# Performance work log

Measured on AMD Instinct MI355X. Metric: run time of the kernel, lower is better.

The kernel has to match this reference:

```python
import jax, jax.numpy as jnp
import numpy as np

H = 768
NH = 12
DH = H // NH  # 64


def setup_inputs() -> dict:
    key = jax.random.key(0)
    ks = jax.random.split(key, 20)
    s = 1.0 / np.sqrt(H)
    def lin(k, din, dout):
        kw, kb = jax.random.split(k)
        W = jax.random.uniform(kw, (din, dout), jnp.float32, -s, s)
        b = jax.random.uniform(kb, (dout,), jnp.float32, -s, s)
        return W, b
    Wq, bq = lin(ks[0], H, H)
    Wk, bk = lin(ks[1], H, H)
    Wv, bv = lin(ks[2], H, H)
    Wt, bt = lin(ks[3], H, H)
    Wi, bi = lin(ks[4], H, H)
    W1, b1 = lin(ks[5], H, H)
    W2, b2 = lin(ks[6], H, 1)
    text = jax.random.normal(ks[7], (8, 64, H), jnp.float32)
    image = jax.random.normal(ks[8], (8, 197, H), jnp.float32)
    return dict(text=text, image=image, Wq=Wq, bq=bq, Wk=Wk, bk=bk, Wv=Wv, bv=bv,
                Wt=Wt, bt=bt, Wi=Wi, bi=bi, W1=W1, b1=b1, W2=W2, b2=b2)


def reference(text, image, Wq, bq, Wk, bk, Wv, bv, Wt, bt, Wi, bi, W1, b1, W2, b2):
    bsz, t_len, _ = text.shape
    i_len = image.shape[1]
    # relevance gate MLP on broadcast product
    text_emb = text @ Wt + bt          # [b, t, H]
    image_emb = image @ Wi + bi        # [b, i, H]
    rel = text_emb[:, :, None, :] * image_emb[:, None, :, :]  # [b, t, i, H]
    rel = jax.nn.relu(rel @ W1 + b1)
    gate = jax.nn.sigmoid(rel @ W2 + b2)  # [b, t, i, 1]
    gate = gate.reshape(bsz, 1, t_len, i_len)
    # cross-attention
    def heads(x, L):
        return x.reshape(bsz, L, NH, DH).transpose(0, 2, 1, 3)  # [b, h, L, dh]
    q = heads(text @ Wq + bq, t_len)
    k = heads(image @ Wk + bk, i_len)
    v = heads(image @ Wv + bv, i_len)
    scores = jnp.einsum('bhtd,bhid->bhti', q, k) / np.sqrt(DH)
    probs = jax.nn.softmax(scores, axis=-1) * gate   # [b, h, t, i]
    ctx = jnp.einsum('bhti,bhid->bhtd', probs, v)    # [b, h, t, dh]
    return ctx.transpose(0, 2, 1, 3).reshape(bsz, t_len, H)
```

## Files before the change

### kernel.cpp

```cpp
#include <hip/hip_runtime.h>
#include <stdint.h>

#define HD 768
#define NHEADS 12
#define DHEAD 64
#define BATCH 8
#define TLEN 64
#define ILEN 197
#define NPAIRS 100864
#define MTILES 394

typedef __attribute__((ext_vector_type(8))) short short8;
typedef __attribute__((ext_vector_type(4))) float f32x4;

__device__ __forceinline__ short f2bf(float x) {
    union { float f; uint32_t u; } v; v.f = x;
    uint32_t r = v.u + 0x7FFFu + ((v.u >> 16) & 1u);
    return (short)(r >> 16);
}
__device__ __forceinline__ float bf2f(short s) {
    union { uint32_t u; float f; } v; v.u = ((uint32_t)(unsigned short)s) << 16;
    return v.f;
}
__device__ __forceinline__ void gll16(const void* g, void* l) {
    __builtin_amdgcn_global_load_lds(
        (const __attribute__((address_space(1))) unsigned int*)g,
        (__attribute__((address_space(3))) unsigned int*)l, 16, 0, 0);
}

__global__ __launch_bounds__(256) void prep_weights(
    const float* __restrict__ Wq, const float* __restrict__ Wk,
    const float* __restrict__ Wv, const float* __restrict__ Wt,
    const float* __restrict__ Wi, const float* __restrict__ W1,
    short* __restrict__ W5s, short* __restrict__ W1Bs)
{
    __shared__ float tile[64][65];
    int bx = blockIdx.x;
    int tid = threadIdx.x;
    if (bx >= 720) {
        int idx = bx - 720;
        int pn = idx / 12, kt = idx - pn * 12;
        int c = tid;
        int j = pn * 256 + c;
        char* dst = (char*)W1Bs + (size_t)idx * 32768 + c * 128;
        int swz = (c & 7) << 4;
#pragma unroll
        for (int kg = 0; kg < 8; ++kg) {
            short8 o;
#pragma unroll
            for (int e = 0; e < 8; ++e)
                o[e] = f2bf(W1[(size_t)(kt * 64 + kg * 8 + e) * HD + j]);
            *(short8*)(dst + ((kg * 16) ^ swz)) = o;
        }
        return;
    }
    int seg = bx / 144, ti = bx - seg * 144;
    const float* src = (seg == 0) ? Wt : (seg == 1) ? Wq : (seg == 2) ? Wi
                     : (seg == 3) ? Wk : Wv;
    int kt = ti / 12, ntile = ti - kt * 12;
#pragma unroll
    for (int pass = 0; pass < 16; ++pass) {
        int idx = pass * 256 + tid;
        int kk = idx >> 6, nn = idx & 63;
        tile[kk][nn] = src[(size_t)(kt * 64 + kk) * HD + ntile * 64 + nn];
    }
    __syncthreads();
    size_t base = ((size_t)(seg * 12 + ntile) * 12 + kt) * 8192;
#pragma unroll
    for (int pass = 0; pass < 16; ++pass) {
        int idx = pass * 256 + tid;
        int col = idx >> 6, kloc = idx & 63;
        float x = tile[kloc][col];
        short h = f2bf(x);
        short lw = f2bf(x - bf2f(h));
        int sidx = (col * 64 + kloc) ^ ((col & 7) << 3);
        W5s[base + sidx] = h;
        W5s[base + 4096 + sidx] = lw;
    }
}

__global__ __launch_bounds__(256, 1) void proj_kernel(
    const float* __restrict__ X, int M,
    const short* __restrict__ W5s, int segbase,
    const float* __restrict__ bias0, const float* __restrict__ bias1,
    const float* __restrict__ bias2,
    float* __restrict__ out0, float* __restrict__ out1, float* __restrict__ out2)
{
    __shared__ __align__(16) short Bs[2][8192];
    int tid = threadIdx.x;
    int l = tid & 63, w = tid >> 6;
    int lo = l & 15, grp = l >> 4;
    int y = blockIdx.y;
    int segl = y / 12, ntile = y - segl * 12;
    int seg = segbase + segl;
    const char* wsrc = (const char*)W5s + (size_t)((seg * 12 + ntile) * 12) * 16384;
    {
        const char* s = wsrc + w * 4096 + l * 16;
        char* d = (char*)&Bs[0][0] + w * 4096;
        gll16(s, d); gll16(s + 1024, d + 1024);
        gll16(s + 2048, d + 2048); gll16(s + 3072, d + 3072);
    }
    int arow = blockIdx.x * 64 + w * 16 + lo;
    bool aok = arow < M;
    const float* xrow = X + (size_t)(aok ? arow : 0) * HD;
    short8 ah[24], al[24];
#pragma unroll
    for (int kc = 0; kc < 24; ++kc) {
        int kb = kc * 32 + grp * 8;
        float4 xa = {0.f, 0.f, 0.f, 0.f}, xb = {0.f, 0.f, 0.f, 0.f};
        if (aok) { xa = *(const float4*)(xrow + kb); xb = *(const float4*)(xrow + kb + 4); }
        float xs[8] = {xa.x, xa.y, xa.z, xa.w, xb.x, xb.y, xb.z, xb.w};
#pragma unroll
        for (int e = 0; e < 8; ++e) {
            short hh = f2bf(xs[e]);
            ah[kc][e] = hh;
            al[kc][e] = f2bf(xs[e] - bf2f(hh));
        }
    }
    __syncthreads();

    f32x4 acc[4];
    f32x4 z4 = {0.f, 0.f, 0.f, 0.f};
#pragma unroll
    for (int js = 0; js < 4; ++js) acc[js] = z4;

#pragma unroll
    for (int kk = 0; kk < 12; ++kk) {
        const short* buf = &Bs[kk & 1][0];
        if (kk < 11) {
            const char* s = wsrc + (size_t)(kk + 1) * 16384 + w * 4096 + l * 16;
            char* d = (char*)&Bs[(kk + 1) & 1][0] + w * 4096;
            gll16(s, d); gll16(s + 1024, d + 1024);
            gll16(s + 2048, d + 2048); gll16(s + 3072, d + 3072);
            asm volatile("s_waitcnt vmcnt(4)" ::: "memory");
        } else {
            asm volatile("s_waitcnt vmcnt(0)" ::: "memory");
        }
        __builtin_amdgcn_s_barrier();
        asm volatile("" ::: "memory");
#pragma unroll
        for (int js = 0; js < 4; ++js) {
            int col = js * 16 + lo;
            int base = col * 64;
            int sw = (col & 7) << 3;
#pragma unroll
            for (int kcl = 0; kcl < 2; ++kcl) {
                int idx = (base + kcl * 32 + grp * 8) ^ sw;
                short8 bh = *(const short8*)&buf[idx];
                short8 bl = *(const short8*)&buf[4096 + idx];
                int kc = kk * 2 + kcl;
                acc[js] = __builtin_amdgcn_mfma_f32_16x16x32_bf16(ah[kc], bh, acc[js], 0, 0, 0);
                acc[js] = __builtin_amdgcn_mfma_f32_16x16x32_bf16(ah[kc], bl, acc[js], 0, 0, 0);
                acc[js] = __builtin_amdgcn_mfma_f32_16x16x32_bf16(al[kc], bh, acc[js], 0, 0, 0);
            }
        }
        asm volatile("s_waitcnt lgkmcnt(0)" ::: "memory");
        __builtin_amdgcn_s_barrier();
        asm volatile("" ::: "memory");
    }
    const float* bp = (segl == 0) ? bias0 : (segl == 1) ? bias1 : bias2;
    float* op = (segl == 0) ? out0 : (segl == 1) ? out1 : out2;
#pragma unroll
    for (int js = 0; js < 4; ++js) {
        int cc = ntile * 64 + js * 16 + lo;
        float bvv = bp[cc];
#pragma unroll
        for (int r = 0; r < 4; ++r) {
            int orow = blockIdx.x * 64 + w * 16 + grp * 4 + r;
            if (orow < M) op[(size_t)orow * HD + cc] = acc[js][r] + bvv;
        }
    }
}

__global__ __launch_bounds__(256) void build_a(
    const float* __restrict__ te, const float* __restrict__ ie,
    short* __restrict__ As, int mstart)
{
    int bx = blockIdx.x;
    int m_l = bx / 12, kt = bx - m_l * 12;
    int tid = threadIdx.x;
    int p = (mstart + m_l) * 256 + tid;
    int b = p / 12608; int rr = p - b * 12608;
    int t = rr / 197;  int i = rr - t * 197;
    const float* tp = te + (size_t)(b * 64 + t) * HD + kt * 64;
    const float* ip = ie + (size_t)(b * 197 + i) * HD + kt * 64;
    char* dst = (char*)As + ((size_t)(m_l * 12 + kt) * 32768) + tid * 128;
    int swz = (tid & 7) << 4;
#pragma unroll
    for (int kg = 0; kg < 8; ++kg) {
        float4 xa = *(const float4*)(ip + kg * 8);
        float4 xb = *(const float4*)(ip + kg * 8 + 4);
        float4 ta = *(const float4*)(tp + kg * 8);
        float4 tb = *(const float4*)(tp + kg * 8 + 4);
        short8 o;
        o[0] = f2bf(xa.x * ta.x); o[1] = f2bf(xa.y * ta.y);
        o[2] = f2bf(xa.z * ta.z); o[3] = f2bf(xa.w * ta.w);
        o[4] = f2bf(xb.x * tb.x); o[5] = f2bf(xb.y * tb.y);
        o[6] = f2bf(xb.z * tb.z); o[7] = f2bf(xb.w * tb.w);
        *(short8*)(dst + ((kg * 16) ^ swz)) = o;
    }
}

__global__ __launch_bounds__(512, 2) void gate_gemm(
    const short* __restrict__ As, const short* __restrict__ W1Bs,
    const float* __restrict__ b1, const float* __restrict__ W2,
    float* __restrict__ plg, int mstart)
{
    __shared__ __align__(16) char lds[131072];
    int tid = threadIdx.x;
    int lane = tid & 63, wid = tid >> 6;
    int lo = lane & 15, grp = lane >> 4;
    int wr = wid >> 2, wc = wid & 2 ? (wid & 3) : (wid & 3);
    wc = wid & 3;
    int bx0 = blockIdx.x;
    int nwg = gridDim.x;
    int qq = nwg >> 3, rr8 = nwg & 7;
    int xcd = bx0 & 7;
    int logical = (xcd < rr8 ? xcd * (qq + 1) : rr8 * (qq + 1) + (xcd - rr8) * qq)
                + (bx0 >> 3);
    int m_l = logical / 3, pn = logical - m_l * 3;

    const char* Ag = (const char*)As + (size_t)m_l * 12 * 32768;
    const char* Bg = (const char*)W1Bs + (size_t)pn * 12 * 32768;

    {
        gll16(Ag + tid * 16,          lds + tid * 16);
        gll16(Ag + 8192 + tid * 16,   lds + 8192 + tid * 16);
        gll16(Ag + 16384 + tid * 16,  lds + 16384 + tid * 16);
        gll16(Ag + 24576 + tid * 16,  lds + 24576 + tid * 16);
        gll16(Bg + tid * 16,          lds + 65536 + tid * 16);
        gll16(Bg + 8192 + tid * 16,   lds + 65536 + 8192 + tid * 16);
        gll16(Bg + 16384 + tid * 16,  lds + 65536 + 16384 + tid * 16);
        gll16(Bg + 24576 + tid * 16,  lds + 65536 + 24576 + tid * 16);
    }

    f32x4 acc[8][4];
    f32x4 z4 = {0.f, 0.f, 0.f, 0.f};
#pragma unroll
    for (int rt = 0; rt < 8; ++rt)
#pragma unroll
        for (int ct = 0; ct < 4; ++ct) acc[rt][ct] = z4;
    int swz = (lo & 7) << 4;

    for (int kt = 0; kt < 12; ++kt) {
        int par = kt & 1, npar = par ^ 1;
        int aoff = par * 32768;
        int boff = 65536 + par * 32768;
        bool more = kt < 11;

        asm volatile("s_waitcnt vmcnt(0)" ::: "memory");
        __builtin_amdgcn_s_barrier();
        asm volatile("" ::: "memory");

        if (more) {
            const char* Aun = Ag + (size_t)(kt + 1) * 32768;
            const char* Bun = Bg + (size_t)(kt + 1) * 32768;
            int dA = npar * 32768, dB = 65536 + npar * 32768;
            gll16(Aun + tid * 16,          lds + dA + tid * 16);
            gll16(Aun + 8192 + tid * 16,   lds + dA + 8192 + tid * 16);
            gll16(Aun + 16384 + tid * 16,  lds + dA + 16384 + tid * 16);
            gll16(Aun + 24576 + tid * 16,  lds + dA + 24576 + tid * 16);
            gll16(Bun + tid * 16,          lds + dB + tid * 16);
            gll16(Bun + 8192 + tid * 16,   lds + dB + 8192 + tid * 16);
            gll16(Bun + 16384 + tid * 16,  lds + dB + 16384 + tid * 16);
            gll16(Bun + 24576 + tid * 16,  lds + dB + 24576 + tid * 16);
        }

        short8 bfr[4][2];
#pragma unroll
        for (int ct = 0; ct < 4; ++ct) {
            int c = wc * 64 + ct * 16 + lo;
#pragma unroll
            for (int ks = 0; ks < 2; ++ks)
                bfr[ct][ks] = *(const short8*)(lds + boff + c * 128 + ((ks * 64 + grp * 16) ^ swz));
        }
#pragma unroll
        for (int q = 0; q < 4; ++q) {
            short8 af[2][2];
#pragma unroll
            for (int i2 = 0; i2 < 2; ++i2) {
                int r = wr * 128 + (2 * q + i2) * 16 + lo;
#pragma unroll
                for (int ks = 0; ks < 2; ++ks)
                    af[i2][ks] = *(const short8*)(lds + aoff + r * 128 + ((ks * 64 + grp * 16) ^ swz));
            }
            __builtin_amdgcn_s_setprio(1);
#pragma unroll
            for (int i2 = 0; i2 < 2; ++i2)
#pragma unroll
                for (int ct = 0; ct < 4; ++ct)
#pragma unroll
                    for (int ks = 0; ks < 2; ++ks)
                        acc[2 * q + i2][ct] = __builtin_amdgcn_mfma_f32_16x16x32_bf16(
                            af[i2][ks], bfr[ct][ks], acc[2 * q + i2][ct], 0, 0, 0);
            __builtin_amdgcn_s_setprio(0);
        }
    }

    float b1v[4], w2v[4];
#pragma unroll
    for (int ct = 0; ct < 4; ++ct) {
        int j = pn * 256 + wc * 64 + ct * 16 + lo;
        b1v[ct] = b1[j]; w2v[ct] = W2[j];
    }
    float pl[8][4];
#pragma unroll
    for (int rt = 0; rt < 8; ++rt)
#pragma unroll
        for (int r = 0; r < 4; ++r) {
            float s = 0.f;
#pragma unroll
            for (int ct = 0; ct < 4; ++ct)
                s += fmaxf(acc[rt][ct][r] + b1v[ct], 0.f) * w2v[ct];
            pl[rt][r] = s;
        }
#pragma unroll
    for (int msk = 1; msk <= 8; msk <<= 1)
#pragma unroll
        for (int rt = 0; rt < 8; ++rt)
#pragma unroll
            for (int r = 0; r < 4; ++r)
                pl[rt][r] += __shfl_xor(pl[rt][r], msk);

    __syncthreads();
    float* red = (float*)lds;
    if (lo == 0) {
#pragma unroll
        for (int rt = 0; rt < 8; ++rt)
#pragma unroll
            for (int r = 0; r < 4; ++r)
                red[wid * 128 + rt * 16 + grp * 4 + r] = pl[rt][r];
    }
    __syncthreads();
    if (tid < 256) {
        int wr_ = tid >> 7, rl = tid & 127;
        float s = red[(wr_ * 4 + 0) * 128 + rl] + red[(wr_ * 4 + 1) * 128 + rl]
                + red[(wr_ * 4 + 2) * 128 + rl] + red[(wr_ * 4 + 3) * 128 + rl];
        plg[(size_t)pn * NPAIRS + (size_t)(mstart + m_l) * 256 + tid] = s;
    }
}

__global__ __launch_bounds__(256) void gate_fin(
    const float* __restrict__ plg, const float* __restrict__ b2,
    float* __restrict__ gateb)
{
    int idx = blockIdx.x * 256 + threadIdx.x;
    if (idx < NPAIRS) {
        float s = plg[idx] + plg[NPAIRS + idx] + plg[2 * NPAIRS + idx] + b2[0];
        gateb[idx] = 1.f / (1.f + __expf(-s));
    }
}

__global__ __launch_bounds__(256) void attn_kernel(
    const float* __restrict__ q, const float* __restrict__ k,
    const float* __restrict__ v, const float* __restrict__ gate,
    float* __restrict__ out)
{
    __shared__ float k_s[ILEN * 65];
    __shared__ float p_s[4][200];
    int bx = blockIdx.x;
    int tq = bx & 3;
    int h = (bx >> 2) % NHEADS;
    int b = bx / (4 * NHEADS);
    int tid = threadIdx.x;
    for (int idx = tid; idx < ILEN * DHEAD; idx += 256) {
        int i = idx >> 6, d = idx & 63;
        k_s[i * 65 + d] = k[(size_t)(b * ILEN + i) * HD + h * DHEAD + d];
    }
    __syncthreads();

    int l = tid & 63, w = tid >> 6;
    for (int tt = 0; tt < 4; ++tt) {
        int t = tq * 16 + w * 4 + tt;
        float qv = q[(size_t)(b * 64 + t) * HD + h * DHEAD + l];
        float s0 = 0.f, s1 = 0.f, s2 = 0.f, s3 = 0.f;
        int i0 = l, i1 = 64 + l, i2 = 128 + l;
        int i3c = (192 + l < ILEN) ? 192 + l : 0;
        for (int d = 0; d < 64; ++d) {
            float qd = __shfl(qv, d);
            s0 += qd * k_s[i0 * 65 + d];
            s1 += qd * k_s[i1 * 65 + d];
            s2 += qd * k_s[i2 * 65 + d];
            s3 += qd * k_s[i3c * 65 + d];
        }
        float sc[4] = {s0, s1, s2, s3};
        float m = -3.0e38f;
#pragma unroll
        for (int rep = 0; rep < 4; ++rep) {
            int i = rep * 64 + l;
            sc[rep] = (i < ILEN) ? sc[rep] * 0.125f : -3.0e38f;
            m = fmaxf(m, sc[rep]);
        }
        for (int mask = 32; mask >= 1; mask >>= 1) m = fmaxf(m, __shfl_xor(m, mask));
        float sum = 0.f;
#pragma unroll
        for (int rep = 0; rep < 4; ++rep) {
            float e = __expf(sc[rep] - m);
            sc[rep] = e;
            sum += e;
        }
        for (int mask = 32; mask >= 1; mask >>= 1) sum += __shfl_xor(sum, mask);
        float inv = 1.f / sum;
        const float* grow = gate + (size_t)(b * 64 + t) * ILEN;
#pragma unroll
        for (int rep = 0; rep < 4; ++rep) {
            int i = rep * 64 + l;
            if (i < 200) p_s[w][i] = (i < ILEN) ? sc[rep] * inv * grow[i] : 0.f;
        }
        float ctx = 0.f;
        const float* vbase = v + (size_t)(b * ILEN) * HD + h * DHEAD + l;
        for (int c = 0; c < 49; ++c) {
            float4 p4 = *(const float4*)&p_s[w][c * 4];
            ctx += p4.x * vbase[(size_t)(c * 4 + 0) * HD];
            ctx += p4.y * vbase[(size_t)(c * 4 + 1) * HD];
            ctx += p4.z * vbase[(size_t)(c * 4 + 2) * HD];
            ctx += p4.w * vbase[(size_t)(c * 4 + 3) * HD];
        }
        {
            float4 p4 = *(const float4*)&p_s[w][196];
            ctx += p4.x * vbase[(size_t)196 * HD];
        }
        out[(size_t)(b * 64 + t) * HD + h * DHEAD + l] = ctx;
    }
}

extern "C" void kernel_launch(void* const* d_in, const int* in_sizes, int n_in,
                              void* d_out, int out_size, void* d_ws, size_t ws_size,
                              hipStream_t stream)
{
    const float* text  = (const float*)d_in[0];
    const float* image = (const float*)d_in[1];
    const float* Wq = (const float*)d_in[2];
    const float* bq = (const float*)d_in[3];
    const float* Wk = (const float*)d_in[4];
    const float* bk = (const float*)d_in[5];
    const float* Wv = (const float*)d_in[6];
    const float* bv = (const float*)d_in[7];
    const float* Wt = (const float*)d_in[8];
    const float* bt = (const float*)d_in[9];
    const float* Wi = (const float*)d_in[10];
    const float* bi = (const float*)d_in[11];
    const float* W1 = (const float*)d_in[12];
    const float* b1 = (const float*)d_in[13];
    const float* W2 = (const float*)d_in[14];
    const float* b2 = (const float*)d_in[15];
    float* out = (float*)d_out;

    char* ws = (char*)d_ws;
    size_t off = 0;
    auto carve = [&](size_t bytes) -> void* {
        void* p = (void*)(ws + off);
        off += (bytes + 255) & ~(size_t)255;
        return p;
    };
    short* W5s  = (short*)carve((size_t)5 * 144 * 8192 * 2);
    short* W1Bs = (short*)carve((size_t)36 * 32768);
    float* te    = (float*)carve((size_t)512 * 768 * 4);
    float* qb    = (float*)carve((size_t)512 * 768 * 4);
    float* ieb   = (float*)carve((size_t)1576 * 768 * 4);
    float* kb    = (float*)carve((size_t)1576 * 768 * 4);
    float* vb    = (float*)carve((size_t)1576 * 768 * 4);
    float* gateb = (float*)carve((size_t)NPAIRS * 4);
    float* plg   = (float*)carve((size_t)3 * NPAIRS * 4);

    size_t per_m = (size_t)12 * 32768;
    size_t avail = (ws_size > off) ? (ws_size - off) : 0;
    int stripe = (int)(avail / per_m);
    if (stripe > MTILES) stripe = MTILES;
    if (stripe < 1) stripe = 1;
    short* As = (short*)(ws + off);
    int nst = (MTILES + stripe - 1) / stripe;

    hipLaunchKernelGGL(prep_weights, dim3(756), dim3(256), 0, stream,
                       Wq, Wk, Wv, Wt, Wi, W1, W5s, W1Bs);
    hipLaunchKernelGGL(proj_kernel, dim3(8, 24), dim3(256), 0, stream,
                       text, 512, W5s, 0, bt, bq, (const float*)nullptr,
                       te, qb, (float*)nullptr);
    hipLaunchKernelGGL(proj_kernel, dim3(25, 36), dim3(256), 0, stream,
                       image, 1576, W5s, 2, bi, bk, bv,
                       ieb, kb, vb);
    for (int s = 0; s < nst; ++s) {
        int m0 = s * stripe;
        int mc = (MTILES - m0 < stripe) ? (MTILES - m0) : stripe;
        hipLaunchKernelGGL(build_a, dim3(mc * 12), dim3(256), 0, stream,
                           te, ieb, As, m0);
        hipLaunchKernelGGL(gate_gemm, dim3(mc * 3), dim3(512), 0, stream,
                           As, W1Bs, b1, W2, plg, m0);
    }
    hipLaunchKernelGGL(gate_fin, dim3((NPAIRS + 255) / 256), dim3(256), 0, stream,
                       plg, b2, gateb);
    hipLaunchKernelGGL(attn_kernel, dim3(BATCH * NHEADS * 4), dim3(256), 0, stream,
                       qb, kb, vb, gateb, out);
}
```

Before: 389.1 us.

## Split gate GEMM K-tiles to 32 and use four-stage LDS prefetch pipeline

The gate GEMM's K tile goes from 64 to 32. The packed A and W1 buffers are re-laid out into 16 KB chunks with a matching 4-way swizzle, and the main loop uses a 4-slot ring buffer with three tiles in flight. Partial vmcnt waits replace the full drain, so global-to-LDS loads overlap with MFMA work instead of blocking each iteration. The trade-off is twice as many barriers, each covering half the MFMA work, plus changed layouts in prep_weights and build_a.

```diff
diff --git a/kernel.cpp b/kernel.cpp
--- a/kernel.cpp
+++ b/kernel.cpp
@@ -39,17 +39,17 @@
     int tid = threadIdx.x;
     if (bx >= 720) {
         int idx = bx - 720;
-        int pn = idx / 12, kt = idx - pn * 12;
+        int pn = idx / 24, kt = idx - pn * 24;
         int c = tid;
         int j = pn * 256 + c;
-        char* dst = (char*)W1Bs + (size_t)idx * 32768 + c * 128;
-        int swz = (c & 7) << 4;
-#pragma unroll
-        for (int kg = 0; kg < 8; ++kg) {
+        char* dst = (char*)W1Bs + (size_t)idx * 16384 + c * 64;
+        int swz = (c & 3) << 4;
+#pragma unroll
+        for (int kg = 0; kg < 4; ++kg) {
             short8 o;
 #pragma unroll
             for (int e = 0; e < 8; ++e)
-                o[e] = f2bf(W1[(size_t)(kt * 64 + kg * 8 + e) * HD + j]);
+                o[e] = f2bf(W1[(size_t)(kt * 32 + kg * 8 + e) * HD + j]);
             *(short8*)(dst + ((kg * 16) ^ swz)) = o;
         }
         return;
@@ -184,20 +184,24 @@
     int t = rr / 197;  int i = rr - t * 197;
     const float* tp = te + (size_t)(b * 64 + t) * HD + kt * 64;
     const float* ip = ie + (size_t)(b * 197 + i) * HD + kt * 64;
-    char* dst = (char*)As + ((size_t)(m_l * 12 + kt) * 32768) + tid * 128;
-    int swz = (tid & 7) << 4;
-#pragma unroll
-    for (int kg = 0; kg < 8; ++kg) {
-        float4 xa = *(const float4*)(ip + kg * 8);
-        float4 xb = *(const float4*)(ip + kg * 8 + 4);
-        float4 ta = *(const float4*)(tp + kg * 8);
-        float4 tb = *(const float4*)(tp + kg * 8 + 4);
-        short8 o;
-        o[0] = f2bf(xa.x * ta.x); o[1] = f2bf(xa.y * ta.y);
-        o[2] = f2bf(xa.z * ta.z); o[3] = f2bf(xa.w * ta.w);
-        o[4] = f2bf(xb.x * tb.x); o[5] = f2bf(xb.y * tb.y);
-        o[6] = f2bf(xb.z * tb.z); o[7] = f2bf(xb.w * tb.w);
-        *(short8*)(dst + ((kg * 16) ^ swz)) = o;
+    int swz = (tid & 3) << 4;
+#pragma unroll
+    for (int h = 0; h < 2; ++h) {
+        char* dst = (char*)As + ((size_t)(m_l * 24 + kt * 2 + h) * 16384) + tid * 64;
+#pragma unroll
+        for (int kg = 0; kg < 4; ++kg) {
+            int kb = h * 32 + kg * 8;
+            float4 xa = *(const float4*)(ip + kb);
+            float4 xb = *(const float4*)(ip + kb + 4);
+            float4 ta = *(const float4*)(tp + kb);
+            float4 tb = *(const float4*)(tp + kb + 4);
+            short8 o;
+            o[0] = f2bf(xa.x * ta.x); o[1] = f2bf(xa.y * ta.y);
+            o[2] = f2bf(xa.z * ta.z); o[3] = f2bf(xa.w * ta.w);
+            o[4] = f2bf(xb.x * tb.x); o[5] = f2bf(xb.y * tb.y);
+            o[6] = f2bf(xb.z * tb.z); o[7] = f2bf(xb.w * tb.w);
+            *(short8*)(dst + ((kg * 16) ^ swz)) = o;
+        }
     }
 }
 
@@ -210,8 +214,7 @@
     int tid = threadIdx.x;
     int lane = tid & 63, wid = tid >> 6;
     int lo = lane & 15, grp = lane >> 4;
-    int wr = wid >> 2, wc = wid & 2 ? (wid & 3) : (wid & 3);
-    wc = wid & 3;
+    int wr = wid >> 2, wc = wid & 3;
     int bx0 = blockIdx.x;
     int nwg = gridDim.x;
     int qq = nwg >> 3, rr8 = nwg & 7;
@@ -220,19 +223,19 @@
                 + (bx0 >> 3);
     int m_l = logical / 3, pn = logical - m_l * 3;
 
-    const char* Ag = (const char*)As + (size_t)m_l * 12 * 32768;
-    const char* Bg = (const char*)W1Bs + (size_t)pn * 12 * 32768;
-
-    {
-        gll16(Ag + tid * 16,          lds + tid * 16);
-        gll16(Ag + 8192 + tid * 16,   lds + 8192 + tid * 16);
-        gll16(Ag + 16384 + tid * 16,  lds + 16384 + tid * 16);
-        gll16(Ag + 24576 + tid * 16,  lds + 24576 + tid * 16);
-        gll16(Bg + tid * 16,          lds + 65536 + tid * 16);
-        gll16(Bg + 8192 + tid * 16,   lds + 65536 + 8192 + tid * 16);
-        gll16(Bg + 16384 + tid * 16,  lds + 65536 + 16384 + tid * 16);
-        gll16(Bg + 24576 + tid * 16,  lds + 65536 + 24576 + tid * 16);
-    }
+    const char* Ag = (const char*)As + (size_t)m_l * 24 * 16384;
+    const char* Bg = (const char*)W1Bs + (size_t)pn * 24 * 16384;
+
+    auto stage = [&](int tt) {
+        int s = (tt & 3) * 16384;
+        const char* sa = Ag + (size_t)tt * 16384 + tid * 16;
+        const char* sb = Bg + (size_t)tt * 16384 + tid * 16;
+        gll16(sa,        lds + s + tid * 16);
+        gll16(sa + 8192, lds + s + 8192 + tid * 16);
+        gll16(sb,        lds + 65536 + s + tid * 16);
+        gll16(sb + 8192, lds + 65536 + s + 8192 + tid * 16);
+    };
+    stage(0); stage(1); stage(2);
 
     f32x4 acc[8][4];
     f32x4 z4 = {0.f, 0.f, 0.f, 0.f};
@@ -240,59 +243,39 @@
     for (int rt = 0; rt < 8; ++rt)
 #pragma unroll
         for (int ct = 0; ct < 4; ++ct) acc[rt][ct] = z4;
-    int swz = (lo & 7) << 4;
-
-    for (int kt = 0; kt < 12; ++kt) {
-        int par = kt & 1, npar = par ^ 1;
-        int aoff = par * 32768;
-        int boff = 65536 + par * 32768;
-        bool more = kt < 11;
-
-        asm volatile("s_waitcnt vmcnt(0)" ::: "memory");
+    int swz = (lo & 3) << 4;
+
+    for (int k = 0; k < 24; ++k) {
+        if (k <= 21)      asm volatile("s_waitcnt vmcnt(8)" ::: "memory");
+        else if (k == 22) asm volatile("s_waitcnt vmcnt(4)" ::: "memory");
+        else              asm volatile("s_waitcnt vmcnt(0)" ::: "memory");
         __builtin_amdgcn_s_barrier();
         asm volatile("" ::: "memory");
-
-        if (more) {
-            const char* Aun = Ag + (size_t)(kt + 1) * 32768;
-            const char* Bun = Bg + (size_t)(kt + 1) * 32768;
-            int dA = npar * 32768, dB = 65536 + npar * 32768;
-            gll16(Aun + tid * 16,          lds + dA + tid * 16);
-            gll16(Aun + 8192 + tid * 16,   lds + dA + 8192 + tid * 16);
-            gll16(Aun + 16384 + tid * 16,  lds + dA + 16384 + tid * 16);
-            gll16(Aun + 24576 + tid * 16,  lds + dA + 24576 + tid * 16);
-            gll16(Bun + tid * 16,          lds + dB + tid * 16);
-            gll16(Bun + 8192 + tid * 16,   lds + dB + 8192 + tid * 16);
-            gll16(Bun + 16384 + tid * 16,  lds + dB + 16384 + tid * 16);
-            gll16(Bun + 24576 + tid * 16,  lds + dB + 24576 + tid * 16);
-        }
-
-        short8 bfr[4][2];
+        if (k + 3 < 24) stage(k + 3);
+
+        int sA = (k & 3) * 16384;
+        int sB = 65536 + (k & 3) * 16384;
+        short8 bfr[4];
 #pragma unroll
         for (int ct = 0; ct < 4; ++ct) {
             int c = wc * 64 + ct * 16 + lo;
-#pragma unroll
-            for (int ks = 0; ks < 2; ++ks)
-                bfr[ct][ks] = *(const short8*)(lds + boff + c * 128 + ((ks * 64 + grp * 16) ^ swz));
+            bfr[ct] = *(const short8*)(lds + sB + c * 64 + ((grp * 16) ^ swz));
         }
 #pragma unroll
         for (int q = 0; q < 4; ++q) {
-            short8 af[2][2];
+            short8 af[2];
 #pragma unroll
             for (int i2 = 0; i2 < 2; ++i2) {
                 int r = wr * 128 + (2 * q + i2) * 16 + lo;
-#pragma unroll
-                for (int ks = 0; ks < 2; ++ks)
-                    af[i2][ks] = *(const short8*)(lds + aoff + r * 128 + ((ks * 64 + grp * 16) ^ swz));
+                af[i2] = *(const short8*)(lds + sA + r * 64 + ((grp * 16) ^ swz));
             }
             __builtin_amdgcn_s_setprio(1);
 #pragma unroll
             for (int i2 = 0; i2 < 2; ++i2)
 #pragma unroll
                 for (int ct = 0; ct < 4; ++ct)
-#pragma unroll
-                    for (int ks = 0; ks < 2; ++ks)
-                        acc[2 * q + i2][ct] = __builtin_amdgcn_mfma_f32_16x16x32_bf16(
-                            af[i2][ks], bfr[ct][ks], acc[2 * q + i2][ct], 0, 0, 0);
+                    acc[2 * q + i2][ct] = __builtin_amdgcn_mfma_f32_16x16x32_bf16(
+                        af[i2], bfr[ct], acc[2 * q + i2][ct], 0, 0, 0);
             __builtin_amdgcn_s_setprio(0);
         }
     }
@@ -454,7 +437,7 @@
         return p;
     };
     short* W5s  = (short*)carve((size_t)5 * 144 * 8192 * 2);
-    short* W1Bs = (short*)carve((size_t)36 * 32768);
+    short* W1Bs = (short*)carve((size_t)72 * 16384);
     float* te    = (float*)carve((size_t)512 * 768 * 4);
     float* qb    = (float*)carve((size_t)512 * 768 * 4);
     float* ieb   = (float*)carve((size_t)1576 * 768 * 4);
@@ -463,7 +446,7 @@
     float* gateb = (float*)carve((size_t)NPAIRS * 4);
     float* plg   = (float*)carve((size_t)3 * NPAIRS * 4);
 
-    size_t per_m = (size_t)12 * 32768;
+    size_t per_m = (size_t)24 * 16384;
     size_t avail = (ws_size > off) ? (ws_size - off) : 0;
     int stripe = (int)(avail / per_m);
     if (stripe > MTILES) stripe = MTILES;
@@ -471,7 +454,7 @@
     short* As = (short*)(ws + off);
     int nst = (MTILES + stripe - 1) / stripe;
 
-    hipLaunchKernelGGL(prep_weights, dim3(756), dim3(256), 0, stream,
+    hipLaunchKernelGGL(prep_weights, dim3(792), dim3(256), 0, stream,
                        Wq, Wk, Wv, Wt, Wi, W1, W5s, W1Bs);
     hipLaunchKernelGGL(proj_kernel, dim3(8, 24), dim3(256), 0, stream,
                        text, 512, W5s, 0, bt, bq, (const float*)nullptr,
```

Result: no change. 390.4 us (+0.3%).

## Interleave gate GEMM prefetch with MFMA phases and batch attention PV over rows

Applied to the files above, without the earlier changes.

In the gate GEMM, the next K-tile's global-to-LDS loads are split into four chunks issued between the four MFMA sub-phases, with extra barriers per sub-phase, so that memory traffic overlaps compute instead of being issued all at once after a full barrier. B fragments are loaded inside the first sub-phase. In the attention kernel, probabilities for the four rows a wave handles are stored together, and a single pass over V accumulates all four context outputs, so each V element is read once instead of four times. The extra barriers per K step may add synchronisation overhead.

```diff
diff --git a/kernel.cpp b/kernel.cpp
--- a/kernel.cpp
+++ b/kernel.cpp
@@ -210,8 +210,7 @@
     int tid = threadIdx.x;
     int lane = tid & 63, wid = tid >> 6;
     int lo = lane & 15, grp = lane >> 4;
-    int wr = wid >> 2, wc = wid & 2 ? (wid & 3) : (wid & 3);
-    wc = wid & 3;
+    int wr = wid >> 2, wc = wid & 3;
     int bx0 = blockIdx.x;
     int nwg = gridDim.x;
     int qq = nwg >> 3, rr8 = nwg & 7;
@@ -233,6 +232,9 @@
         gll16(Bg + 16384 + tid * 16,  lds + 65536 + 16384 + tid * 16);
         gll16(Bg + 24576 + tid * 16,  lds + 65536 + 24576 + tid * 16);
     }
+    asm volatile("s_waitcnt vmcnt(0)" ::: "memory");
+    __builtin_amdgcn_s_barrier();
+    asm volatile("" ::: "memory");
 
     f32x4 acc[8][4];
     f32x4 z4 = {0.f, 0.f, 0.f, 0.f};
@@ -247,33 +249,11 @@
         int aoff = par * 32768;
         int boff = 65536 + par * 32768;
         bool more = kt < 11;
-
-        asm volatile("s_waitcnt vmcnt(0)" ::: "memory");
-        __builtin_amdgcn_s_barrier();
-        asm volatile("" ::: "memory");
-
-        if (more) {
-            const char* Aun = Ag + (size_t)(kt + 1) * 32768;
-            const char* Bun = Bg + (size_t)(kt + 1) * 32768;
-            int dA = npar * 32768, dB = 65536 + npar * 32768;
-            gll16(Aun + tid * 16,          lds + dA + tid * 16);
-            gll16(Aun + 8192 + tid * 16,   lds + dA + 8192 + tid * 16);
-            gll16(Aun + 16384 + tid * 16,  lds + dA + 16384 + tid * 16);
-            gll16(Aun + 24576 + tid * 16,  lds + dA + 24576 + tid * 16);
-            gll16(Bun + tid * 16,          lds + dB + tid * 16);
-            gll16(Bun + 8192 + tid * 16,   lds + dB + 8192 + tid * 16);
-            gll16(Bun + 16384 + tid * 16,  lds + dB + 16384 + tid * 16);
-            gll16(Bun + 24576 + tid * 16,  lds + dB + 24576 + tid * 16);
-        }
+        const char* Aun = Ag + (size_t)(kt + 1) * 32768;
+        const char* Bun = Bg + (size_t)(kt + 1) * 32768;
+        int dA = npar * 32768, dB = 65536 + npar * 32768;
 
         short8 bfr[4][2];
-#pragma unroll
-        for (int ct = 0; ct < 4; ++ct) {
-            int c = wc * 64 + ct * 16 + lo;
-#pragma unroll
-            for (int ks = 0; ks < 2; ++ks)
-                bfr[ct][ks] = *(const short8*)(lds + boff + c * 128 + ((ks * 64 + grp * 16) ^ swz));
-        }
 #pragma unroll
         for (int q = 0; q < 4; ++q) {
             short8 af[2][2];
@@ -284,6 +264,32 @@
                 for (int ks = 0; ks < 2; ++ks)
                     af[i2][ks] = *(const short8*)(lds + aoff + r * 128 + ((ks * 64 + grp * 16) ^ swz));
             }
+            if (q == 0) {
+#pragma unroll
+                for (int ct = 0; ct < 4; ++ct) {
+                    int c = wc * 64 + ct * 16 + lo;
+#pragma unroll
+                    for (int ks = 0; ks < 2; ++ks)
+                        bfr[ct][ks] = *(const short8*)(lds + boff + c * 128 + ((ks * 64 + grp * 16) ^ swz));
+                }
+            }
+            if (more) {
+                if (q < 2) {
+                    gll16(Aun + (size_t)(q * 2) * 8192 + tid * 16,
+                          lds + dA + (q * 2) * 8192 + tid * 16);
+                    gll16(Aun + (size_t)(q * 2 + 1) * 8192 + tid * 16,
+                          lds + dA + (q * 2 + 1) * 8192 + tid * 16);
+                } else {
+                    gll16(Bun + (size_t)((q - 2) * 2) * 8192 + tid * 16,
+                          lds + dB + ((q - 2) * 2) * 8192 + tid * 16);
+                    gll16(Bun + (size_t)((q - 2) * 2 + 1) * 8192 + tid * 16,
+                          lds + dB + ((q - 2) * 2 + 1) * 8192 + tid * 16);
+                }
+            }
+            asm volatile("" ::: "memory");
+            __builtin_amdgcn_s_barrier();
+            asm volatile("s_waitcnt lgkmcnt(0)" ::: "memory");
+            __builtin_amdgcn_sched_barrier(0);
             __builtin_amdgcn_s_setprio(1);
 #pragma unroll
             for (int i2 = 0; i2 < 2; ++i2)
@@ -294,6 +300,11 @@
                         acc[2 * q + i2][ct] = __builtin_amdgcn_mfma_f32_16x16x32_bf16(
                             af[i2][ks], bfr[ct][ks], acc[2 * q + i2][ct], 0, 0, 0);
             __builtin_amdgcn_s_setprio(0);
+            if (q == 3) {
+                asm volatile("s_waitcnt vmcnt(0)" ::: "memory");
+            }
+            __builtin_amdgcn_s_barrier();
+            asm volatile("" ::: "memory");
         }
     }
 
@@ -357,7 +368,7 @@
     float* __restrict__ out)
 {
     __shared__ float k_s[ILEN * 65];
-    __shared__ float p_s[4][200];
+    __shared__ float p_s[4][ILEN][4];
     int bx = blockIdx.x;
     int tq = bx & 3;
     int h = (bx >> 2) % NHEADS;
@@ -370,8 +381,10 @@
     __syncthreads();
 
     int l = tid & 63, w = tid >> 6;
+    int tbase = tq * 16 + w * 4;
+
     for (int tt = 0; tt < 4; ++tt) {
-        int t = tq * 16 + w * 4 + tt;
+        int t = tbase + tt;
         float qv = q[(size_t)(b * 64 + t) * HD + h * DHEAD + l];
         float s0 = 0.f, s1 = 0.f, s2 = 0.f, s3 = 0.f;
         int i0 = l, i1 = 64 + l, i2 = 128 + l;
@@ -405,23 +418,24 @@
 #pragma unroll
         for (int rep = 0; rep < 4; ++rep) {
             int i = rep * 64 + l;
-            if (i < 200) p_s[w][i] = (i < ILEN) ? sc[rep] * inv * grow[i] : 0.f;
-        }
-        float ctx = 0.f;
-        const float* vbase = v + (size_t)(b * ILEN) * HD + h * DHEAD + l;
-        for (int c = 0; c < 49; ++c) {
-            float4 p4 = *(const float4*)&p_s[w][c * 4];
-            ctx += p4.x * vbase[(size_t)(c * 4 + 0) * HD];
-            ctx += p4.y * vbase[(size_t)(c * 4 + 1) * HD];
-            ctx += p4.z * vbase[(size_t)(c * 4 + 2) * HD];
-            ctx += p4.w * vbase[(size_t)(c * 4 + 3) * HD];
-        }
-        {
-            float4 p4 = *(const float4*)&p_s[w][196];
-            ctx += p4.x * vbase[(size_t)196 * HD];
-        }
-        out[(size_t)(b * 64 + t) * HD + h * DHEAD + l] = ctx;
-    }
+            if (i < ILEN) p_s[w][i][tt] = sc[rep] * inv * grow[i];
+        }
+    }
+
+    float ctx[4] = {0.f, 0.f, 0.f, 0.f};
+    const float* vbase = v + (size_t)(b * ILEN) * HD + h * DHEAD + l;
+#pragma unroll 4
+    for (int i = 0; i < ILEN; ++i) {
+        float vv = vbase[(size_t)i * HD];
+        float4 p4 = *(const float4*)&p_s[w][i][0];
+        ctx[0] += p4.x * vv;
+        ctx[1] += p4.y * vv;
+        ctx[2] += p4.z * vv;
+        ctx[3] += p4.w * vv;
+    }
+#pragma unroll
+    for (int tt = 0; tt < 4; ++tt)
+        out[(size_t)(b * 64 + tbase + tt) * HD + h * DHEAD + l] = ctx[tt];
 }
 
 extern "C" void kernel_launch(void* const* d_in, const int* in_sizes, int n_in,
```

Measured after the change: 346.6 us. 1.12x faster.
